# Optimization experiments

Measured on AMD Instinct MI355X. Metric: run time of the kernel, lower is better.

## Reference

```python
import jax, jax.numpy as jnp
import numpy as np
from jax import lax

D_MODEL = 512; D_FF = 2048
D_STATE = 16; D_CONV = 4; EXPAND = 2          # mamba_ssm defaults
D_INNER = EXPAND * D_MODEL                    # 1024
DT_RANK = (D_MODEL + 15) // 16                # 32
B, W, C, D = 2, 1024, 64, 8                   # C*D == D_MODEL


def setup_inputs():
    key = jax.random.key(0)
    ks = jax.random.split(key, 24)
    def p(k, shape, s=0.02):
        return jax.random.normal(k, shape, jnp.float32) * s
    inp = {"x": jax.random.normal(ks[0], (B, W, C, D), jnp.float32)}
    for i, pref in enumerate(["fm", "bm"]):
        o = 1 + i * 7
        inp[pref + "_in_W"] = p(ks[o], (2 * D_INNER, D_MODEL))
        inp[pref + "_conv_W"] = p(ks[o + 1], (D_INNER, D_CONV))
        inp[pref + "_conv_b"] = jnp.zeros((D_INNER,), jnp.float32)
        inp[pref + "_xproj_W"] = p(ks[o + 2], (DT_RANK + 2 * D_STATE, D_INNER))
        inp[pref + "_dt_W"] = p(ks[o + 3], (D_INNER, DT_RANK))
        inp[pref + "_dt_b"] = p(ks[o + 4], (D_INNER,), 0.1)
        inp[pref + "_A_log"] = jnp.log(jnp.broadcast_to(
            jnp.arange(1, D_STATE + 1, dtype=jnp.float32), (D_INNER, D_STATE)))
        inp[pref + "_D"] = jnp.ones((D_INNER,), jnp.float32)
        inp[pref + "_out_W"] = p(ks[o + 5], (D_MODEL, D_INNER))
    inp["ln1_g"] = jnp.ones((D_MODEL,), jnp.float32); inp["ln1_b"] = jnp.zeros((D_MODEL,), jnp.float32)
    inp["ln2_g"] = jnp.ones((D_MODEL,), jnp.float32); inp["ln2_b"] = jnp.zeros((D_MODEL,), jnp.float32)
    inp["ln3_g"] = jnp.ones((D_MODEL,), jnp.float32); inp["ln3_b"] = jnp.zeros((D_MODEL,), jnp.float32)
    inp["ff_W1"] = p(ks[15], (D_FF, D_MODEL)); inp["ff_b1"] = jnp.zeros((D_FF,), jnp.float32)
    inp["ff_W2"] = p(ks[16], (D_MODEL, D_FF)); inp["ff_b2"] = jnp.zeros((D_MODEL,), jnp.float32)
    return inp


def _silu(x):
    return x * jax.nn.sigmoid(x)


def _layernorm(x, g, b, eps=1e-5):
    mu = jnp.mean(x, -1, keepdims=True)
    var = jnp.var(x, -1, keepdims=True)
    return (x - mu) * lax.rsqrt(var + eps) * g + b


def _mamba(u, in_W, conv_W, conv_b, xproj_W, dt_W, dt_b, A_log, Dp, out_W):
    # u: (B, L, d_model). Standard Mamba block (mamba_ssm reference math).
    xz = jnp.einsum('bld,ed->ble', u, in_W)            # (B, L, 2*d_inner)
    xm, z = jnp.split(xz, 2, axis=-1)
    # causal depthwise conv along L
    xc = lax.conv_general_dilated(
        xm.transpose(0, 2, 1), conv_W[:, None, :], (1,),
        [(D_CONV - 1, 0)], feature_group_count=D_INNER)
    xm = _silu((xc + conv_b[None, :, None]).transpose(0, 2, 1))  # (B, L, d_inner)
    dbc = jnp.einsum('bld,ed->ble', xm, xproj_W)       # (B, L, dt_rank + 2*d_state)
    dt = dbc[..., :DT_RANK]
    Bm = dbc[..., DT_RANK:DT_RANK + D_STATE]           # (B, L, d_state)
    Cm = dbc[..., DT_RANK + D_STATE:]                  # (B, L, d_state)
    delta = jax.nn.softplus(jnp.einsum('blr,dr->bld', dt, dt_W) + dt_b)  # (B, L, d_inner)
    A = -jnp.exp(A_log)                                # (d_inner, d_state)
    dA = jnp.exp(delta[..., None] * A)                 # (B, L, d_inner, d_state)
    dBu = delta[..., None] * Bm[:, :, None, :] * xm[..., None]

    def step(h, inputs):
        dA_t, dBu_t = inputs
        h = dA_t * h + dBu_t
        return h, h

    h0 = jnp.zeros((u.shape[0], D_INNER, D_STATE), u.dtype)
    _, hs = lax.scan(step, h0, (dA.transpose(1, 0, 2, 3), dBu.transpose(1, 0, 2, 3)))
    y = jnp.einsum('lbds,lbs->bld', hs, Cm.transpose(1, 0, 2))
    y = y + xm * Dp
    y = y * _silu(z)
    return jnp.einsum('ble,de->bld', y, out_W)         # (B, L, d_model)


def reference(x,
              fm_in_W, fm_conv_W, fm_conv_b, fm_xproj_W, fm_dt_W, fm_dt_b, fm_A_log, fm_D, fm_out_W,
              bm_in_W, bm_conv_W, bm_conv_b, bm_xproj_W, bm_dt_W, bm_dt_b, bm_A_log, bm_D, bm_out_W,
              ln1_g, ln1_b, ln2_g, ln2_b, ln3_g, ln3_b,
              ff_W1, ff_b1, ff_W2, ff_b2):
    b, w, c, d = x.shape
    xf = x.reshape(b, w, c * d)
    fwd = _mamba(xf, fm_in_W, fm_conv_W, fm_conv_b, fm_xproj_W, fm_dt_W, fm_dt_b, fm_A_log, fm_D, fm_out_W)
    bwd = jnp.flip(_mamba(jnp.flip(xf, 1), bm_in_W, bm_conv_W, bm_conv_b, bm_xproj_W,
                          bm_dt_W, bm_dt_b, bm_A_log, bm_D, bm_out_W), 1)
    an1 = _layernorm(xf + fwd, ln1_g, ln1_b)   # AddNorm: LN(x + dropout(y)); dropout off at eval
    an2 = _layernorm(xf + bwd, ln2_g, ln2_b)
    out = an1 + an2
    h = jnp.maximum(jnp.einsum('bld,fd->blf', out, ff_W1) + ff_b1, 0)
    ff = jnp.einsum('blf,df->bld', h, ff_W2) + ff_b2
    out = _layernorm(ff + ff, ln3_g, ln3_b)    # an3(out, out) == LN(out + out)
    return out.reshape(b, w, c, d)
```

## Files before the change

### kernel.cpp

```cpp
#include <hip/hip_runtime.h>
#include <hip/hip_bf16.h>
#include <math.h>

#define MM 2048
#define BATCH 2
#define SEQ 1024
#define DMODEL 512
#define DINNER 1024
#define DSTATE 16
#define DTRANK 32
#define DFF 2048

#define NCHUNK 16
#define CHUNK 64
#define GTOT 65536

typedef short bf16x8 __attribute__((ext_vector_type(8)));
typedef float floatx4 __attribute__((ext_vector_type(4)));
typedef unsigned short ushort8v __attribute__((ext_vector_type(8)));
typedef unsigned short ushort4v __attribute__((ext_vector_type(4)));

__device__ __forceinline__ unsigned short f2bf(float f) {
    union { float f; unsigned u; } v; v.f = f;
    unsigned r = v.u + 0x7FFF + ((v.u >> 16) & 1);
    return (unsigned short)(r >> 16);
}
__device__ __forceinline__ float bf2f(unsigned short u) {
    union { unsigned u; float f; } v; v.u = ((unsigned)u) << 16; return v.f;
}

__device__ __forceinline__ float rowsum16(float x) {
    union { float f; int i; } a, b;
    a.f = x;
    b.i = __builtin_amdgcn_update_dpp(0, a.i, 0x128, 0xF, 0xF, false); a.f += b.f;
    b.i = __builtin_amdgcn_update_dpp(0, a.i, 0x124, 0xF, 0xF, false); a.f += b.f;
    b.i = __builtin_amdgcn_update_dpp(0, a.i, 0x122, 0xF, 0xF, false); a.f += b.f;
    b.i = __builtin_amdgcn_update_dpp(0, a.i, 0x121, 0xF, 0xF, false); a.f += b.f;
    return a.f;
}

#define GLOAD_LDS16(gp, lp) __builtin_amdgcn_global_load_lds( \
    (const __attribute__((address_space(1))) unsigned int*)(gp), \
    (__attribute__((address_space(3))) unsigned int*)(lp), 16, 0, 0)

template<int EPI, int OUTBF16>
__global__ __launch_bounds__(256) void gemm_mfma_batch(
    int M, int N, int K,
    const unsigned short* __restrict__ A0, const unsigned short* __restrict__ A1, int lda,
    const unsigned short* __restrict__ B0, const unsigned short* __restrict__ B1, int ldb,
    const float* __restrict__ bias,
    void* __restrict__ C0, void* __restrict__ C1, int ldc)
{
    __shared__ unsigned short As[128 * 32];
    __shared__ unsigned short Bs[128 * 32];
    const int z = blockIdx.z;
    const unsigned short* A = z ? A1 : A0;
    const unsigned short* B = z ? B1 : B0;
    void* Cout = z ? C1 : C0;
    const int tid  = threadIdx.x;
    const int wave = tid >> 6;
    const int lane = tid & 63;
    const int bm = blockIdx.y * 128;
    const int bn = blockIdx.x * 128;

    const int strow = lane & 15;
    const int stkc  = lane >> 4;
    const int wr = wave >> 1, wc = wave & 1;
    const int frow = lane & 15;
    const int fkc  = lane >> 4;

    floatx4 acc[4][4];
    #pragma unroll
    for (int i = 0; i < 4; ++i)
        #pragma unroll
        for (int j = 0; j < 4; ++j)
            acc[i][j] = (floatx4){0.f, 0.f, 0.f, 0.f};

    for (int k0 = 0; k0 < K; k0 += 32) {
        __syncthreads();
        #pragma unroll
        for (int q = 0; q < 2; ++q) {
            int g = wave * 2 + q;
            GLOAD_LDS16(A + (size_t)(bm + g * 16 + strow) * lda + k0 + stkc * 8,
                        As + g * 512);
        }
        #pragma unroll
        for (int q = 0; q < 2; ++q) {
            int g = wave * 2 + q;
            GLOAD_LDS16(B + (size_t)(bn + g * 16 + strow) * ldb + k0 + stkc * 8,
                        Bs + g * 512);
        }
        __syncthreads();

        bf16x8 af[4], bfr[4];
        #pragma unroll
        for (int i = 0; i < 4; ++i)
            af[i] = *(const bf16x8*)(As + (wr * 4 + i) * 512 + fkc * 128 + frow * 8);
        #pragma unroll
        for (int j = 0; j < 4; ++j)
            bfr[j] = *(const bf16x8*)(Bs + (wc * 4 + j) * 512 + fkc * 128 + frow * 8);
        #pragma unroll
        for (int i = 0; i < 4; ++i)
            #pragma unroll
            for (int j = 0; j < 4; ++j)
                acc[i][j] = __builtin_amdgcn_mfma_f32_16x16x32_bf16(
                    af[i], bfr[j], acc[i][j], 0, 0, 0);
    }

    const int orow0 = bm + wr * 64 + (lane >> 4) * 4;
    const int ocol0 = bn + wc * 64 + (lane & 15);
    #pragma unroll
    for (int j = 0; j < 4; ++j) {
        const int col = ocol0 + j * 16;
        const float bv = bias ? bias[col] : 0.f;
        #pragma unroll
        for (int i = 0; i < 4; ++i) {
            #pragma unroll
            for (int r = 0; r < 4; ++r) {
                int row = orow0 + i * 16 + r;
                float t = acc[i][j][r] + bv;
                if (EPI == 1) t = fmaxf(t, 0.f);
                if (OUTBF16)
                    ((unsigned short*)Cout)[(size_t)row * ldc + col] = f2bf(t);
                else
                    ((float*)Cout)[(size_t)row * ldc + col] = t;
            }
        }
    }
}

__global__ __launch_bounds__(256) void gemm_inproj_kernel(
    const unsigned short* __restrict__ A,
    const unsigned short* __restrict__ B0, const unsigned short* __restrict__ B1,
    float* __restrict__ Cx0, float* __restrict__ Cz0,
    float* __restrict__ Cx1, float* __restrict__ Cz1)
{
    __shared__ unsigned short As[128 * 32];
    __shared__ unsigned short Bs[128 * 32];
    const int z = blockIdx.z;
    const unsigned short* B = z ? B1 : B0;
    const int tid  = threadIdx.x;
    const int wave = tid >> 6;
    const int lane = tid & 63;
    const int bm = blockIdx.y * 128;
    const int bn = blockIdx.x * 128;

    const int strow = lane & 15;
    const int stkc  = lane >> 4;
    const int wr = wave >> 1, wc = wave & 1;
    const int frow = lane & 15;
    const int fkc  = lane >> 4;

    floatx4 acc[4][4];
    #pragma unroll
    for (int i = 0; i < 4; ++i)
        #pragma unroll
        for (int j = 0; j < 4; ++j)
            acc[i][j] = (floatx4){0.f, 0.f, 0.f, 0.f};

    for (int k0 = 0; k0 < DMODEL; k0 += 32) {
        __syncthreads();
        #pragma unroll
        for (int q = 0; q < 2; ++q) {
            int g = wave * 2 + q;
            GLOAD_LDS16(A + (size_t)(bm + g * 16 + strow) * DMODEL + k0 + stkc * 8,
                        As + g * 512);
        }
        #pragma unroll
        for (int q = 0; q < 2; ++q) {
            int g = wave * 2 + q;
            GLOAD_LDS16(B + (size_t)(bn + g * 16 + strow) * DMODEL + k0 + stkc * 8,
                        Bs + g * 512);
        }
        __syncthreads();

        bf16x8 af[4], bfr[4];
        #pragma unroll
        for (int i = 0; i < 4; ++i)
            af[i] = *(const bf16x8*)(As + (wr * 4 + i) * 512 + fkc * 128 + frow * 8);
        #pragma unroll
        for (int j = 0; j < 4; ++j)
            bfr[j] = *(const bf16x8*)(Bs + (wc * 4 + j) * 512 + fkc * 128 + frow * 8);
        #pragma unroll
        for (int i = 0; i < 4; ++i)
            #pragma unroll
            for (int j = 0; j < 4; ++j)
                acc[i][j] = __builtin_amdgcn_mfma_f32_16x16x32_bf16(
                    af[i], bfr[j], acc[i][j], 0, 0, 0);
    }

    const int zh = bn >= DINNER;
    float* C = z ? (zh ? Cz1 : Cx1) : (zh ? Cz0 : Cx0);
    const int cb = zh ? DINNER : 0;
    const int orow0 = bm + wr * 64 + (lane >> 4) * 4;
    const int ocol0 = bn + wc * 64 + (lane & 15) - cb;
    #pragma unroll
    for (int j = 0; j < 4; ++j) {
        const int col = ocol0 + j * 16;
        #pragma unroll
        for (int i = 0; i < 4; ++i)
            #pragma unroll
            for (int r = 0; r < 4; ++r)
                C[(size_t)(orow0 + i * 16 + r) * DINNER + col] = acc[i][j][r];
    }
}

template<int NSPLIT>
__global__ __launch_bounds__(256) void gemm_mfma_splitk(
    int M, int N, int K,
    const unsigned short* __restrict__ A0, const unsigned short* __restrict__ A1, int lda,
    const unsigned short* __restrict__ B0, const unsigned short* __restrict__ B1, int ldb,
    float* __restrict__ part, int ldc)
{
    __shared__ unsigned short As[128 * 32];
    __shared__ unsigned short Bs[128 * 32];
    const int z = blockIdx.z;
    const int dir = z / NSPLIT, sp = z % NSPLIT;
    const unsigned short* A = dir ? A1 : A0;
    const unsigned short* B = dir ? B1 : B0;
    float* Cp = part + (size_t)z * M * ldc;
    const int kbeg = sp * (K / NSPLIT);
    const int kend = kbeg + (K / NSPLIT);
    const int tid  = threadIdx.x;
    const int wave = tid >> 6;
    const int lane = tid & 63;
    const int bm = blockIdx.y * 128;
    const int bn = blockIdx.x * 128;

    const int strow = lane & 15;
    const int stkc  = lane >> 4;
    const int wr = wave >> 1, wc = wave & 1;
    const int frow = lane & 15;
    const int fkc  = lane >> 4;

    floatx4 acc[4][4];
    #pragma unroll
    for (int i = 0; i < 4; ++i)
        #pragma unroll
        for (int j = 0; j < 4; ++j)
            acc[i][j] = (floatx4){0.f, 0.f, 0.f, 0.f};

    for (int k0 = kbeg; k0 < kend; k0 += 32) {
        __syncthreads();
        #pragma unroll
        for (int q = 0; q < 2; ++q) {
            int g = wave * 2 + q;
            GLOAD_LDS16(A + (size_t)(bm + g * 16 + strow) * lda + k0 + stkc * 8,
                        As + g * 512);
        }
        #pragma unroll
        for (int q = 0; q < 2; ++q) {
            int g = wave * 2 + q;
            GLOAD_LDS16(B + (size_t)(bn + g * 16 + strow) * ldb + k0 + stkc * 8,
                        Bs + g * 512);
        }
        __syncthreads();

        bf16x8 af[4], bfr[4];
        #pragma unroll
        for (int i = 0; i < 4; ++i)
            af[i] = *(const bf16x8*)(As + (wr * 4 + i) * 512 + fkc * 128 + frow * 8);
        #pragma unroll
        for (int j = 0; j < 4; ++j)
            bfr[j] = *(const bf16x8*)(Bs + (wc * 4 + j) * 512 + fkc * 128 + frow * 8);
        #pragma unroll
        for (int i = 0; i < 4; ++i)
            #pragma unroll
            for (int j = 0; j < 4; ++j)
                acc[i][j] = __builtin_amdgcn_mfma_f32_16x16x32_bf16(
                    af[i], bfr[j], acc[i][j], 0, 0, 0);
    }

    const int orow0 = bm + wr * 64 + (lane >> 4) * 4;
    const int ocol0 = bn + wc * 64 + (lane & 15);
    #pragma unroll
    for (int j = 0; j < 4; ++j) {
        const int col = ocol0 + j * 16;
        #pragma unroll
        for (int i = 0; i < 4; ++i)
            #pragma unroll
            for (int r = 0; r < 4; ++r)
                Cp[(size_t)(orow0 + i * 16 + r) * ldc + col] = acc[i][j][r];
    }
}

__global__ __launch_bounds__(256) void reduce_splitk_kernel(
    const float* __restrict__ part, int nsplit, int elems, int ldc,
    const float* __restrict__ bias, float* __restrict__ out)
{
    int i = (blockIdx.x * 256 + threadIdx.x) * 4;
    if (i >= elems) return;
    float4 a = *(const float4*)(part + i);
    for (int s = 1; s < nsplit; ++s) {
        float4 t = *(const float4*)(part + (size_t)s * elems + i);
        a.x += t.x; a.y += t.y; a.z += t.z; a.w += t.w;
    }
    if (bias) {
        int c = i % ldc;
        a.x += bias[c]; a.y += bias[c + 1]; a.z += bias[c + 2]; a.w += bias[c + 3];
    }
    *(float4*)(out + i) = a;
}

__global__ __launch_bounds__(256) void reduce_splitk2_dual_kernel(
    const float* __restrict__ part, float* __restrict__ out0, float* __restrict__ out1)
{
    const int dir = blockIdx.y;
    const int i = (blockIdx.x * 256 + threadIdx.x) * 4;
    const float* p = part + (size_t)dir * 2 * (MM * DMODEL);
    float4 a = *(const float4*)(p + i);
    float4 t = *(const float4*)(p + (size_t)(MM * DMODEL) + i);
    a.x += t.x; a.y += t.y; a.z += t.z; a.w += t.w;
    float* out = dir ? out1 : out0;
    *(float4*)(out + i) = a;
}

__global__ __launch_bounds__(256) void xproj_splitk_kernel(
    const unsigned short* __restrict__ A_f, const unsigned short* __restrict__ A_b,
    const unsigned short* __restrict__ Wf,  const unsigned short* __restrict__ Wb,
    float* __restrict__ part)
{
    __shared__ unsigned short As[128 * 32];
    __shared__ unsigned short Bs[64 * 32];
    const int tid = threadIdx.x, wave = tid >> 6, lane = tid & 63;
    const int bm = blockIdx.x * 128;
    const int dir = blockIdx.y >> 2, sp = blockIdx.y & 3;
    const unsigned short* A = dir ? A_b : A_f;
    const unsigned short* W = dir ? Wb  : Wf;
    float* Cp = part + (size_t)blockIdx.y * MM * 64;
    const int kbeg = sp * 256, kend = kbeg + 256;

    const int strow = lane & 15;
    const int stkc  = lane >> 4;
    const int frow = lane & 15;
    const int fkc  = lane >> 4;

    floatx4 acc[2][4];
    #pragma unroll
    for (int i = 0; i < 2; ++i)
        #pragma unroll
        for (int j = 0; j < 4; ++j)
            acc[i][j] = (floatx4){0.f, 0.f, 0.f, 0.f};

    for (int k0 = kbeg; k0 < kend; k0 += 32) {
        __syncthreads();
        #pragma unroll
        for (int q = 0; q < 2; ++q) {
            int g = wave * 2 + q;
            GLOAD_LDS16(A + (size_t)(bm + g * 16 + strow) * DINNER + k0 + stkc * 8,
                        As + g * 512);
        }
        GLOAD_LDS16(W + (size_t)(wave * 16 + strow) * DINNER + k0 + stkc * 8,
                    Bs + wave * 512);
        __syncthreads();

        bf16x8 af[2], bfr[4];
        #pragma unroll
        for (int i = 0; i < 2; ++i)
            af[i] = *(const bf16x8*)(As + (wave * 2 + i) * 512 + fkc * 128 + frow * 8);
        #pragma unroll
        for (int j = 0; j < 4; ++j)
            bfr[j] = *(const bf16x8*)(Bs + j * 512 + fkc * 128 + frow * 8);
        #pragma unroll
        for (int i = 0; i < 2; ++i)
            #pragma unroll
            for (int j = 0; j < 4; ++j)
                acc[i][j] = __builtin_amdgcn_mfma_f32_16x16x32_bf16(
                    af[i], bfr[j], acc[i][j], 0, 0, 0);
    }

    const int orow0 = bm + wave * 32 + (lane >> 4) * 4;
    #pragma unroll
    for (int j = 0; j < 4; ++j) {
        const int col = (lane & 15) + j * 16;
        #pragma unroll
        for (int i = 0; i < 2; ++i)
            #pragma unroll
            for (int r = 0; r < 4; ++r)
                Cp[(size_t)(orow0 + i * 16 + r) * 64 + col] = acc[i][j][r];
    }
}

__global__ __launch_bounds__(256) void xproj_reduce_kernel(
    const float* __restrict__ part,
    float* __restrict__ dbc_f, float* __restrict__ dbc_b,
    float* __restrict__ dbcT_f, float* __restrict__ dbcT_b)
{
    const int dir = blockIdx.y;
    const int i = (blockIdx.x * 256 + threadIdx.x) * 4;
    const float* p = part + (size_t)dir * 4 * (MM * 64);
    float4 a = *(const float4*)(p + i);
    #pragma unroll
    for (int s = 1; s < 4; ++s) {
        float4 t = *(const float4*)(p + (size_t)s * (MM * 64) + i);
        a.x += t.x; a.y += t.y; a.z += t.z; a.w += t.w;
    }
    float* dbc  = dir ? dbc_b  : dbc_f;
    float* dbcT = dir ? dbcT_b : dbcT_f;
    *(float4*)(dbc + i) = a;
    const int m = i >> 6, c = i & 63;
    dbcT[(size_t)(c + 0) * MM + m] = a.x;
    dbcT[(size_t)(c + 1) * MM + m] = a.y;
    dbcT[(size_t)(c + 2) * MM + m] = a.z;
    dbcT[(size_t)(c + 3) * MM + m] = a.w;
}

__global__ __launch_bounds__(256) void dtproj_batch_kernel(
    int M, int N, int K,
    const float* __restrict__ A0, const float* __restrict__ A1, int lda,
    const float* __restrict__ B0, const float* __restrict__ B1, int ldb,
    const float* __restrict__ bias0, const float* __restrict__ bias1,
    unsigned short* __restrict__ C0, unsigned short* __restrict__ C1, int ldc)
{
    __shared__ float As[16][64];
    __shared__ float Bs[16][64];
    const int z = blockIdx.z;
    const float* A = z ? A1 : A0;
    const float* B = z ? B1 : B0;
    const float* biasR = z ? bias1 : bias0;
    unsigned short* C = z ? C1 : C0;
    const int tid = threadIdx.x;
    const int tx = tid & 15, ty = tid >> 4;
    const int bm = blockIdx.y * 64, bn = blockIdx.x * 64;
    const int lm = tid & 63;
    const int lk = (tid >> 6) * 4;
    const float* Arow = A + (size_t)(bm + lm) * lda + lk;
    const float* Brow = B + (size_t)(bn + lm) * ldb + lk;
    float acc[4][4] = {};
    for (int k0 = 0; k0 < K; k0 += 16) {
        float4 av = *(const float4*)(Arow + k0);
        float4 bv = *(const float4*)(Brow + k0);
        __syncthreads();
        As[lk+0][lm] = av.x; As[lk+1][lm] = av.y; As[lk+2][lm] = av.z; As[lk+3][lm] = av.w;
        Bs[lk+0][lm] = bv.x; Bs[lk+1][lm] = bv.y; Bs[lk+2][lm] = bv.z; Bs[lk+3][lm] = bv.w;
        __syncthreads();
        #pragma unroll
        for (int k = 0; k < 16; ++k) {
            float4 a = *(const float4*)(&As[k][ty*4]);
            float4 b = *(const float4*)(&Bs[k][tx*4]);
            float ar[4] = {a.x,a.y,a.z,a.w};
            float br[4] = {b.x,b.y,b.z,b.w};
            #pragma unroll
            for (int i = 0; i < 4; ++i)
                #pragma unroll
                for (int j = 0; j < 4; ++j)
                    acc[i][j] = fmaf(ar[i], br[j], acc[i][j]);
        }
    }
    const int row0 = bm + ty*4, col0 = bn + tx*4;
    #pragma unroll
    for (int i = 0; i < 4; ++i) {
        float br = biasR[row0 + i];
        ushort4v o;
        #pragma unroll
        for (int j = 0; j < 4; ++j) {
            float t = acc[i][j] + br;
            o[j] = f2bf(fmaxf(t, 0.f) + log1pf(__expf(-fabsf(t))));
        }
        *(ushort4v*)(C + (size_t)(row0 + i) * ldc + col0) = o;
    }
}

__global__ __launch_bounds__(256) void cast_pre_kernel(
    const float* __restrict__ x, const float* __restrict__ w0,
    const float* __restrict__ w1, const float* __restrict__ xp0,
    const float* __restrict__ xp1, unsigned short* __restrict__ dst)
{
    int i = (blockIdx.x * 256 + threadIdx.x) * 8;
    const float* src; int off;
    if      (i < 1048576) { src = x;   off = 0; }
    else if (i < 2097152) { src = w0;  off = 1048576; }
    else if (i < 3145728) { src = w1;  off = 2097152; }
    else if (i < 3211264) { src = xp0; off = 3145728; }
    else                  { src = xp1; off = 3211264; }
    float4 a = *(const float4*)(src + i - off);
    float4 b = *(const float4*)(src + i - off + 4);
    ushort8v o;
    o[0] = f2bf(a.x); o[1] = f2bf(a.y); o[2] = f2bf(a.z); o[3] = f2bf(a.w);
    o[4] = f2bf(b.x); o[5] = f2bf(b.y); o[6] = f2bf(b.z); o[7] = f2bf(b.w);
    *(ushort8v*)(dst + i) = o;
}

__global__ __launch_bounds__(256) void cast_post_kernel(
    const float* __restrict__ w0, const float* __restrict__ w1,
    const float* __restrict__ w2, const float* __restrict__ w3,
    unsigned short* __restrict__ dst)
{
    int i = (blockIdx.x * 256 + threadIdx.x) * 8;
    const float* src; int off;
    if      (i < 524288)  { src = w0; off = 0; }
    else if (i < 1048576) { src = w1; off = 524288; }
    else if (i < 2097152) { src = w2; off = 1048576; }
    else                  { src = w3; off = 2097152; }
    float4 a = *(const float4*)(src + i - off);
    float4 b = *(const float4*)(src + i - off + 4);
    ushort8v o;
    o[0] = f2bf(a.x); o[1] = f2bf(a.y); o[2] = f2bf(a.z); o[3] = f2bf(a.w);
    o[4] = f2bf(b.x); o[5] = f2bf(b.y); o[6] = f2bf(b.z); o[7] = f2bf(b.w);
    *(ushort8v*)(dst + i) = o;
}

__global__ __launch_bounds__(256) void conv_silu_kernel(
    const float* __restrict__ x_f, const float* __restrict__ x_b,
    const float* __restrict__ Wf,  const float* __restrict__ Wb,
    const float* __restrict__ cbf, const float* __restrict__ cbb,
    unsigned short* __restrict__ of, unsigned short* __restrict__ ob)
{
    const int dir = blockIdx.y;
    const float* xo = dir ? x_b : x_f;
    const float* convW = dir ? Wb : Wf;
    const float* convb = dir ? cbb : cbf;
    unsigned short* xm_bf = dir ? ob : of;
    int gid = blockIdx.x * 256 + threadIdx.x;
    int c = gid & (DINNER - 1);
    int m = gid >> 10;
    int b = m >> 10;
    int l = m & (SEQ - 1);
    float4 wv = *(const float4*)(convW + c * 4);
    float w[4] = {wv.x, wv.y, wv.z, wv.w};
    float acc = convb[c];
    #pragma unroll
    for (int j = 0; j < 4; ++j) {
        int p = dir ? (l + 3 - j) : (l - 3 + j);
        if (p >= 0 && p < SEQ)
            acc = fmaf(xo[(size_t)(b * SEQ + p) * DINNER + c], w[j], acc);
    }
    float sig = 1.f / (1.f + __expf(-acc));
    xm_bf[(size_t)m * DINNER + c] = f2bf(acc * sig);
}

__global__ __launch_bounds__(256) void transpose_bf16_kernel(
    const unsigned short* __restrict__ in0, const unsigned short* __restrict__ in1,
    unsigned short* __restrict__ out0, unsigned short* __restrict__ out1,
    int R, int C)
{
    __shared__ unsigned short t[32][34];
    const unsigned short* in = blockIdx.z ? in1 : in0;
    unsigned short* out = blockIdx.z ? out1 : out0;
    const int c0 = blockIdx.x * 32, r0 = blockIdx.y * 32;
    const int tx = threadIdx.x & 31, ty = threadIdx.x >> 5;
    #pragma unroll
    for (int rr = 0; rr < 32; rr += 8)
        t[ty + rr][tx] = in[(size_t)(r0 + ty + rr) * C + c0 + tx];
    __syncthreads();
    #pragma unroll
    for (int rr = 0; rr < 32; rr += 8)
        out[(size_t)(c0 + ty + rr) * R + r0 + tx] = t[tx][ty + rr];
}

template<int DIR>
__device__ __forceinline__ void pass1_body(
    const unsigned short* __restrict__ deltaT, const unsigned short* __restrict__ xmT,
    const float* __restrict__ dbcT, const float* __restrict__ Alog,
    const float* __restrict__ Dv,
    float* __restrict__ y0T, float* __restrict__ cumT,
    float* __restrict__ Pout, float* __restrict__ Hout)
{
    const int tid = threadIdx.x;
    const int s = tid & 15;
    const int dloc = tid >> 4;
    const int d = blockIdx.x * 16 + dloc;
    const int b = blockIdx.y / NCHUNK;
    const int c = blockIdx.y % NCHUNK;

    const float A  = -__expf(Alog[d * DSTATE + s]);
    const float Dp = Dv[d];
    const unsigned short* dRow = deltaT + (size_t)d * MM + b * SEQ;
    const unsigned short* xRow = xmT + (size_t)d * MM + b * SEQ;
    const float* bRow = dbcT + (size_t)(DTRANK + s) * MM + b * SEQ;
    const float* cRow = dbcT + (size_t)(DTRANK + DSTATE + s) * MM + b * SEQ;
    float* yRow = y0T + (size_t)d * MM + b * SEQ;
    float* uRow = cumT + (size_t)d * MM + b * SEQ;

    float h = 0.f, sdl = 0.f;
    const int segBase = DIR ? (SEQ - CHUNK - c * CHUNK) : (c * CHUNK);
    for (int ii = 0; ii < CHUNK; ii += 8) {
        const int off = DIR ? (segBase + (CHUNK - 8) - ii) : (segBase + ii);
        ushort8v dl8 = *(const ushort8v*)(dRow + off);
        ushort8v x8  = *(const ushort8v*)(xRow + off);
        float4 b0 = *(const float4*)(bRow + off);
        float4 b1 = *(const float4*)(bRow + off + 4);
        float4 c0 = *(const float4*)(cRow + off);
        float4 c1 = *(const float4*)(cRow + off + 4);
        float Bv[8] = {b0.x,b0.y,b0.z,b0.w,b1.x,b1.y,b1.z,b1.w};
        float Cv[8] = {c0.x,c0.y,c0.z,c0.w,c1.x,c1.y,c1.z,c1.w};
        float yv[8], cu[8];
        #pragma unroll
        for (int u = 0; u < 8; ++u) {
            const int t = DIR ? (7 - u) : u;
            float dlv = bf2f(dl8[t]);
            float xv  = bf2f(x8[t]);
            float dA = __expf(dlv * A);
            sdl += dlv;
            h = fmaf(dA, h, dlv * Bv[t] * xv);
            float part = rowsum16(h * Cv[t]);
            yv[t] = fmaf(xv, Dp, part);
            cu[t] = sdl;
        }
        if (s == 0) {
            *(float4*)(yRow + off)     = (float4){yv[0], yv[1], yv[2], yv[3]};
            *(float4*)(yRow + off + 4) = (float4){yv[4], yv[5], yv[6], yv[7]};
            *(float4*)(uRow + off)     = (float4){cu[0], cu[1], cu[2], cu[3]};
            *(float4*)(uRow + off + 4) = (float4){cu[4], cu[5], cu[6], cu[7]};
        }
    }
    const int g = ((DIR * BATCH + b) * DINNER + d) * DSTATE + s;
    Pout[(size_t)c * GTOT + g] = __expf(sdl * A);
    Hout[(size_t)c * GTOT + g] = h;
}

__global__ __launch_bounds__(256) void scan_pass1_kernel(
    const unsigned short* __restrict__ dT_f, const unsigned short* __restrict__ dT_b,
    const unsigned short* __restrict__ xT_f, const unsigned short* __restrict__ xT_b,
    const float* __restrict__ dbcT_f, const float* __restrict__ dbcT_b,
    const float* __restrict__ Alog_f, const float* __restrict__ Alog_b,
    const float* __restrict__ D_f, const float* __restrict__ D_b,
    float* __restrict__ y0T_f, float* __restrict__ y0T_b,
    float* __restrict__ cumT_f, float* __restrict__ cumT_b,
    float* __restrict__ Pout, float* __restrict__ Hout)
{
    if (blockIdx.z == 0)
        pass1_body<0>(dT_f, xT_f, dbcT_f, Alog_f, D_f, y0T_f, cumT_f, Pout, Hout);
    else
        pass1_body<1>(dT_b, xT_b, dbcT_b, Alog_b, D_b, y0T_b, cumT_b, Pout, Hout);
}

__global__ __launch_bounds__(256) void scan_carry_kernel(
    const float* __restrict__ P, const float* __restrict__ H,
    float* __restrict__ carry)
{
    const int g = blockIdx.x * 256 + threadIdx.x;
    float h = 0.f;
    #pragma unroll
    for (int c = 0; c < NCHUNK; ++c) {
        carry[(size_t)c * GTOT + g] = h;
        h = fmaf(P[(size_t)c * GTOT + g], h, H[(size_t)c * GTOT + g]);
    }
}

__global__ __launch_bounds__(256) void scan_correct_kernel(
    const float* __restrict__ y0T_f, const float* __restrict__ y0T_b,
    const float* __restrict__ cumT_f, const float* __restrict__ cumT_b,
    const float* __restrict__ dbcT_f, const float* __restrict__ dbcT_b,
    const float* __restrict__ Alog_f, const float* __restrict__ Alog_b,
    const float* __restrict__ carry,
    const float* __restrict__ z_f, const float* __restrict__ z_b,
    unsigned short* __restrict__ ybf_f, unsigned short* __restrict__ ybf_b)
{
    __shared__ float Cs[16][33];
    __shared__ float Asm[32][16];
    __shared__ float Cy[32][16];
    __shared__ float t[32][33];

    const int dir = blockIdx.z;
    const float* y0T  = dir ? y0T_b  : y0T_f;
    const float* cumT = dir ? cumT_b : cumT_f;
    const float* dbcT = dir ? dbcT_b : dbcT_f;
    const float* Alog = dir ? Alog_b : Alog_f;
    const float* zon  = dir ? z_b    : z_f;
    unsigned short* ybf = dir ? ybf_b : ybf_f;

    const int m0 = blockIdx.x * 32, d0 = blockIdx.y * 32;
    const int b = m0 >> 10;
    const int l0 = m0 & (SEQ - 1);
    const int c = dir ? ((SEQ - 1 - l0) >> 6) : (l0 >> 6);

    for (int idx = threadIdx.x; idx < 512; idx += 256) {
        int s = idx >> 5, ml = idx & 31;
        Cs[s][ml] = dbcT[(size_t)(DTRANK + DSTATE + s) * MM + m0 + ml];
        int dl2 = idx >> 4, s2 = idx & 15;
        Asm[dl2][s2] = -__expf(Alog[(d0 + dl2) * DSTATE + s2]);
        Cy[dl2][s2] = carry[(size_t)c * GTOT
            + ((size_t)(dir * BATCH + b) * DINNER + d0 + dl2) * DSTATE + s2];
    }
    __syncthreads();

    const int tx = threadIdx.x & 31, ty = threadIdx.x >> 5;
    #pragma unroll
    for (int rr = 0; rr < 32; rr += 8) {
        const int dloc = ty + rr;
        const size_t base = (size_t)(d0 + dloc) * MM + m0 + tx;
        float u  = cumT[base];
        float y0 = y0T[base];
        float corr = 0.f;
        #pragma unroll
        for (int s = 0; s < DSTATE; ++s)
            corr = fmaf(Cs[s][tx] * Cy[dloc][s], __expf(Asm[dloc][s] * u), corr);
        t[dloc][tx] = y0 + corr;
    }
    __syncthreads();
    #pragma unroll
    for (int rr = 0; rr < 32; rr += 8) {
        int m = m0 + ty + rr, d = d0 + tx;
        float z = zon[(size_t)m * DINNER + d];
        float sig = 1.f / (1.f + __expf(-z));
        ybf[(size_t)m * DINNER + d] = f2bf(t[tx][ty + rr] * (z * sig));
    }
}

__global__ __launch_bounds__(256) void ln_combine_kernel(
    const float* __restrict__ xf,
    const float* __restrict__ pf, const float* __restrict__ pb,
    const float* __restrict__ g1, const float* __restrict__ b1,
    const float* __restrict__ g2, const float* __restrict__ b2,
    unsigned short* __restrict__ out)
{
    const int m = blockIdx.x;
    const int tid = threadIdx.x;
    const float* xr = xf + (size_t)m * DMODEL;
    const float* p1 = pf + (size_t)m * DMODEL;
    const float* p2 = pb + (size_t)m * DMODEL;
    float v1a = xr[tid] + p1[tid];
    float v1b = xr[tid + 256] + p1[tid + 256];
    float v2a = xr[tid] + p2[tid];
    float v2b = xr[tid + 256] + p2[tid + 256];
    float s1 = v1a + v1b, q1 = v1a*v1a + v1b*v1b;
    float s2 = v2a + v2b, q2 = v2a*v2a + v2b*v2b;
    #pragma unroll
    for (int off = 32; off; off >>= 1) {
        s1 += __shfl_xor(s1, off); q1 += __shfl_xor(q1, off);
        s2 += __shfl_xor(s2, off); q2 += __shfl_xor(q2, off);
    }
    __shared__ float sm[4][4];
    const int w = tid >> 6;
    if ((tid & 63) == 0) { sm[w][0] = s1; sm[w][1] = q1; sm[w][2] = s2; sm[w][3] = q2; }
    __syncthreads();
    s1 = sm[0][0] + sm[1][0] + sm[2][0] + sm[3][0];
    q1 = sm[0][1] + sm[1][1] + sm[2][1] + sm[3][1];
    s2 = sm[0][2] + sm[1][2] + sm[2][2] + sm[3][2];
    q2 = sm[0][3] + sm[1][3] + sm[2][3] + sm[3][3];
    const float inv = 1.f / DMODEL;
    float mu1 = s1 * inv, mu2 = s2 * inv;
    float rs1 = rsqrtf(q1 * inv - mu1 * mu1 + 1e-5f);
    float rs2 = rsqrtf(q2 * inv - mu2 * mu2 + 1e-5f);
    unsigned short* orow = out + (size_t)m * DMODEL;
    orow[tid]       = f2bf((v1a - mu1) * rs1 * g1[tid]       + b1[tid]
                         + (v2a - mu2) * rs2 * g2[tid]       + b2[tid]);
    orow[tid + 256] = f2bf((v1b - mu1) * rs1 * g1[tid + 256] + b1[tid + 256]
                         + (v2b - mu2) * rs2 * g2[tid + 256] + b2[tid + 256]);
}

__global__ __launch_bounds__(256) void ln_final_kernel(
    const float* __restrict__ ff,
    const float* __restrict__ g, const float* __restrict__ b,
    float* __restrict__ out)
{
    const int m = blockIdx.x;
    const int tid = threadIdx.x;
    const float* fr = ff + (size_t)m * DMODEL;
    float va = 2.f * fr[tid];
    float vb = 2.f * fr[tid + 256];
    float s = va + vb, q = va*va + vb*vb;
    #pragma unroll
    for (int off = 32; off; off >>= 1) {
        s += __shfl_xor(s, off); q += __shfl_xor(q, off);
    }
    __shared__ float sm[4][2];
    const int w = tid >> 6;
    if ((tid & 63) == 0) { sm[w][0] = s; sm[w][1] = q; }
    __syncthreads();
    s = sm[0][0] + sm[1][0] + sm[2][0] + sm[3][0];
    q = sm[0][1] + sm[1][1] + sm[2][1] + sm[3][1];
    const float inv = 1.f / DMODEL;
    float mu = s * inv;
    float rs = rsqrtf(q * inv - mu * mu + 1e-5f);
    float* orow = out + (size_t)m * DMODEL;
    orow[tid]       = (va - mu) * rs * g[tid]       + b[tid];
    orow[tid + 256] = (vb - mu) * rs * g[tid + 256] + b[tid + 256];
}

extern "C" void kernel_launch(void* const* d_in, const int* in_sizes, int n_in,
                              void* d_out, int out_size, void* d_ws, size_t ws_size,
                              hipStream_t stream)
{
    const float* x         = (const float*)d_in[0];
    const float* fm_in_W   = (const float*)d_in[1];
    const float* fm_conv_W = (const float*)d_in[2];
    const float* fm_conv_b = (const float*)d_in[3];
    const float* fm_xproj_W= (const float*)d_in[4];
    const float* fm_dt_W   = (const float*)d_in[5];
    const float* fm_dt_b   = (const float*)d_in[6];
    const float* fm_A_log  = (const float*)d_in[7];
    const float* fm_D      = (const float*)d_in[8];
    const float* fm_out_W  = (const float*)d_in[9];
    const float* bm_in_W   = (const float*)d_in[10];
    const float* bm_conv_W = (const float*)d_in[11];
    const float* bm_conv_b = (const float*)d_in[12];
    const float* bm_xproj_W= (const float*)d_in[13];
    const float* bm_dt_W   = (const float*)d_in[14];
    const float* bm_dt_b   = (const float*)d_in[15];
    const float* bm_A_log  = (const float*)d_in[16];
    const float* bm_D      = (const float*)d_in[17];
    const float* bm_out_W  = (const float*)d_in[18];
    const float* ln1_g     = (const float*)d_in[19];
    const float* ln1_b     = (const float*)d_in[20];
    const float* ln2_g     = (const float*)d_in[21];
    const float* ln2_b     = (const float*)d_in[22];
    const float* ln3_g     = (const float*)d_in[23];
    const float* ln3_b     = (const float*)d_in[24];
    const float* ff_W1     = (const float*)d_in[25];
    const float* ff_b1     = (const float*)d_in[26];
    const float* ff_W2     = (const float*)d_in[27];
    const float* ff_b2     = (const float*)d_in[28];
    float* out = (float*)d_out;

    float* ws = (float*)d_ws;
    size_t o = 0;
    float* xonly_f = ws + o; o += (size_t)MM * DINNER;
    float* xonly_b = ws + o; o += (size_t)MM * DINNER;
    float* zonly_f = ws + o; o += (size_t)MM * DINNER;
    float* zonly_b = ws + o; o += (size_t)MM * DINNER;
    unsigned short* xm_bf_f = (unsigned short*)(ws + o); o += (size_t)MM * DINNER / 2;
    unsigned short* xm_bf_b = (unsigned short*)(ws + o); o += (size_t)MM * DINNER / 2;
    unsigned short* xmT_f   = (unsigned short*)(ws + o); o += (size_t)MM * DINNER / 2;
    unsigned short* xmT_b   = (unsigned short*)(ws + o); o += (size_t)MM * DINNER / 2;
    unsigned short* deltaT_f= (unsigned short*)(ws + o); o += (size_t)MM * DINNER / 2;
    unsigned short* deltaT_b= (unsigned short*)(ws + o); o += (size_t)MM * DINNER / 2;
    float* dbc_f    = ws + o; o += (size_t)MM * 64;
    float* dbc_b    = ws + o; o += (size_t)MM * 64;
    float* dbcT_f   = ws + o; o += (size_t)MM * 64;
    float* dbcT_b   = ws + o; o += (size_t)MM * 64;
    float* y0T_f    = ws + o; o += (size_t)MM * DINNER;
    float* y0T_b    = ws + o; o += (size_t)MM * DINNER;
    float* scanP    = ws + o; o += (size_t)NCHUNK * (GTOT / 16) * 16;
    float* scanH    = ws + o; o += (size_t)NCHUNK * (GTOT / 16) * 16;
    float* scanCy   = ws + o; o += (size_t)NCHUNK * (GTOT / 16) * 16;

    float* cumT_f = xonly_f;
    float* cumT_b = xonly_b;
    unsigned short* x_bf       = (unsigned short*)scanP;
    unsigned short* fm_inW_bf  = x_bf + 1048576;
    unsigned short* bm_inW_bf  = fm_inW_bf + 1048576;
    unsigned short* fm_xpW_bf  = bm_inW_bf + 1048576;
    unsigned short* bm_xpW_bf  = fm_xpW_bf + 65536;
    float* gpartX = y0T_f;
    unsigned short* ybf_f = (unsigned short*)scanP;
    unsigned short* ybf_b = (unsigned short*)scanH;
    unsigned short* fm_outW_bf = (unsigned short*)zonly_f;
    unsigned short* bm_outW_bf = fm_outW_bf + 524288;
    unsigned short* W1_bf      = bm_outW_bf + 524288;
    unsigned short* W2_bf      = W1_bf + 1048576;
    float* gpartO = y0T_f;
    float* proj_f = scanCy;
    float* proj_b = xonly_f;
    unsigned short* outsum_bf  = (unsigned short*)xonly_b;
    unsigned short* h_bf = (unsigned short*)deltaT_f;
    float* ff2 = scanP;

    cast_pre_kernel<<<3276800 / 2048, 256, 0, stream>>>(
        x, fm_in_W, bm_in_W, fm_xproj_W, bm_xproj_W, x_bf);

    gemm_inproj_kernel<<<dim3(2048/128, MM/128, 2), 256, 0, stream>>>(
        x_bf, fm_inW_bf, bm_inW_bf, xonly_f, zonly_f, xonly_b, zonly_b);

    conv_silu_kernel<<<dim3((MM * DINNER) / 256, 2), 256, 0, stream>>>(
        xonly_f, xonly_b, fm_conv_W, bm_conv_W, fm_conv_b, bm_conv_b, xm_bf_f, xm_bf_b);
    transpose_bf16_kernel<<<dim3(DINNER/32, MM/32, 2), 256, 0, stream>>>(
        xm_bf_f, xm_bf_b, xmT_f, xmT_b, MM, DINNER);

    xproj_splitk_kernel<<<dim3(MM/128, 8), 256, 0, stream>>>(
        xm_bf_f, xm_bf_b, fm_xpW_bf, bm_xpW_bf, gpartX);
    xproj_reduce_kernel<<<dim3((MM*64)/1024, 2), 256, 0, stream>>>(
        gpartX, dbc_f, dbc_b, dbcT_f, dbcT_b);

    dtproj_batch_kernel<<<dim3(MM/64, DINNER/64, 2), 256, 0, stream>>>(
        DINNER, MM, DTRANK, fm_dt_W, bm_dt_W, DTRANK, dbc_f, dbc_b, 64,
        fm_dt_b, bm_dt_b, deltaT_f, deltaT_b, MM);

    scan_pass1_kernel<<<dim3(DINNER/16, BATCH*NCHUNK, 2), 256, 0, stream>>>(
        deltaT_f, deltaT_b, xmT_f, xmT_b, dbcT_f, dbcT_b,
        fm_A_log, bm_A_log, fm_D, bm_D,
        y0T_f, y0T_b, cumT_f, cumT_b, scanP, scanH);
    scan_carry_kernel<<<GTOT/256, 256, 0, stream>>>(scanP, scanH, scanCy);
    scan_correct_kernel<<<dim3(MM/32, DINNER/32, 2), 256, 0, stream>>>(
        y0T_f, y0T_b, cumT_f, cumT_b, dbcT_f, dbcT_b, fm_A_log, bm_A_log,
        scanCy, zonly_f, zonly_b, ybf_f, ybf_b);

    cast_post_kernel<<<3145728 / 2048, 256, 0, stream>>>(
        fm_out_W, bm_out_W, ff_W1, ff_W2, fm_outW_bf);

    gemm_mfma_splitk<2><<<dim3(DMODEL/128, MM/128, 4), 256, 0, stream>>>(
        MM, DMODEL, DINNER, ybf_f, ybf_b, DINNER, fm_outW_bf, bm_outW_bf, DINNER,
        gpartO, DMODEL);
    reduce_splitk2_dual_kernel<<<dim3((MM*DMODEL)/1024, 2), 256, 0, stream>>>(
        gpartO, proj_f, proj_b);

    ln_combine_kernel<<<MM, 256, 0, stream>>>(
        x, proj_f, proj_b, ln1_g, ln1_b, ln2_g, ln2_b, outsum_bf);

    gemm_mfma_batch<1,1><<<dim3(DFF/128, MM/128, 1), 256, 0, stream>>>(
        MM, DFF, DMODEL, outsum_bf, outsum_bf, DMODEL, W1_bf, W1_bf, DMODEL,
        ff_b1, h_bf, h_bf, DFF);

    gemm_mfma_splitk<4><<<dim3(DMODEL/128, MM/128, 4), 256, 0, stream>>>(
        MM, DMODEL, DFF, h_bf, h_bf, DFF, W2_bf, W2_bf, DFF, gpartO, DMODEL);
    reduce_splitk_kernel<<<(MM*DMODEL)/1024, 256, 0, stream>>>(
        gpartO, 4, MM*DMODEL, DMODEL, ff_b2, ff2);

    ln_final_kernel<<<MM, 256, 0, stream>>>(ff2, ln3_g, ln3_b, out);
}
```

Baseline: 365.1 us.

## Fuse split-K reductions into layernorms, store y0 as bf16, repack B/C row-major

Both split-K reduce kernels are removed. The layernorm kernels now sum the partial GEMM outputs directly from a dedicated workspace, which saves two launches and a full write and read of the intermediate. The x-proj reduce writes delta-rank and B/C as separate row-major arrays instead of a strided transposed copy, so the scan kernels read B/C per timestep with stride 32. The scan's intermediate y0 is also stored in bf16 to halve that traffic, at some cost in precision.

```diff
diff --git a/kernel.cpp b/kernel.cpp
--- a/kernel.cpp
+++ b/kernel.cpp
@@ -284,37 +284,6 @@
     }
 }
 
-__global__ __launch_bounds__(256) void reduce_splitk_kernel(
-    const float* __restrict__ part, int nsplit, int elems, int ldc,
-    const float* __restrict__ bias, float* __restrict__ out)
-{
-    int i = (blockIdx.x * 256 + threadIdx.x) * 4;
-    if (i >= elems) return;
-    float4 a = *(const float4*)(part + i);
-    for (int s = 1; s < nsplit; ++s) {
-        float4 t = *(const float4*)(part + (size_t)s * elems + i);
-        a.x += t.x; a.y += t.y; a.z += t.z; a.w += t.w;
-    }
-    if (bias) {
-        int c = i % ldc;
-        a.x += bias[c]; a.y += bias[c + 1]; a.z += bias[c + 2]; a.w += bias[c + 3];
-    }
-    *(float4*)(out + i) = a;
-}
-
-__global__ __launch_bounds__(256) void reduce_splitk2_dual_kernel(
-    const float* __restrict__ part, float* __restrict__ out0, float* __restrict__ out1)
-{
-    const int dir = blockIdx.y;
-    const int i = (blockIdx.x * 256 + threadIdx.x) * 4;
-    const float* p = part + (size_t)dir * 2 * (MM * DMODEL);
-    float4 a = *(const float4*)(p + i);
-    float4 t = *(const float4*)(p + (size_t)(MM * DMODEL) + i);
-    a.x += t.x; a.y += t.y; a.z += t.z; a.w += t.w;
-    float* out = dir ? out1 : out0;
-    *(float4*)(out + i) = a;
-}
-
 __global__ __launch_bounds__(256) void xproj_splitk_kernel(
     const unsigned short* __restrict__ A_f, const unsigned short* __restrict__ A_b,
     const unsigned short* __restrict__ Wf,  const unsigned short* __restrict__ Wb,
@@ -384,7 +353,7 @@
 __global__ __launch_bounds__(256) void xproj_reduce_kernel(
     const float* __restrict__ part,
     float* __restrict__ dbc_f, float* __restrict__ dbc_b,
-    float* __restrict__ dbcT_f, float* __restrict__ dbcT_b)
+    float* __restrict__ bct_f, float* __restrict__ bct_b)
 {
     const int dir = blockIdx.y;
     const int i = (blockIdx.x * 256 + threadIdx.x) * 4;
@@ -395,14 +364,14 @@
         float4 t = *(const float4*)(p + (size_t)s * (MM * 64) + i);
         a.x += t.x; a.y += t.y; a.z += t.z; a.w += t.w;
     }
-    float* dbc  = dir ? dbc_b  : dbc_f;
-    float* dbcT = dir ? dbcT_b : dbcT_f;
-    *(float4*)(dbc + i) = a;
     const int m = i >> 6, c = i & 63;
-    dbcT[(size_t)(c + 0) * MM + m] = a.x;
-    dbcT[(size_t)(c + 1) * MM + m] = a.y;
-    dbcT[(size_t)(c + 2) * MM + m] = a.z;
-    dbcT[(size_t)(c + 3) * MM + m] = a.w;
+    if (c < 32) {
+        float* dbc = dir ? dbc_b : dbc_f;
+        *(float4*)(dbc + (size_t)m * 32 + c) = a;
+    } else {
+        float* bct = dir ? bct_b : bct_f;
+        *(float4*)(bct + (size_t)m * 32 + (c - 32)) = a;
+    }
 }
 
 __global__ __launch_bounds__(256) void dtproj_batch_kernel(
@@ -551,9 +520,9 @@
 template<int DIR>
 __device__ __forceinline__ void pass1_body(
     const unsigned short* __restrict__ deltaT, const unsigned short* __restrict__ xmT,
-    const float* __restrict__ dbcT, const float* __restrict__ Alog,
+    const float* __restrict__ bct, const float* __restrict__ Alog,
     const float* __restrict__ Dv,
-    float* __restrict__ y0T, float* __restrict__ cumT,
+    unsigned short* __restrict__ y0T, float* __restrict__ cumT,
     float* __restrict__ Pout, float* __restrict__ Hout)
 {
     const int tid = threadIdx.x;
@@ -567,9 +536,8 @@
     const float Dp = Dv[d];
     const unsigned short* dRow = deltaT + (size_t)d * MM + b * SEQ;
     const unsigned short* xRow = xmT + (size_t)d * MM + b * SEQ;
-    const float* bRow = dbcT + (size_t)(DTRANK + s) * MM + b * SEQ;
-    const float* cRow = dbcT + (size_t)(DTRANK + DSTATE + s) * MM + b * SEQ;
-    float* yRow = y0T + (size_t)d * MM + b * SEQ;
+    const float* bcRow = bct + (size_t)(b * SEQ) * 32 + s;
+    unsigned short* yRow = y0T + (size_t)d * MM + b * SEQ;
     float* uRow = cumT + (size_t)d * MM + b * SEQ;
 
     float h = 0.f, sdl = 0.f;
@@ -578,12 +546,13 @@
         const int off = DIR ? (segBase + (CHUNK - 8) - ii) : (segBase + ii);
         ushort8v dl8 = *(const ushort8v*)(dRow + off);
         ushort8v x8  = *(const ushort8v*)(xRow + off);
-        float4 b0 = *(const float4*)(bRow + off);
-        float4 b1 = *(const float4*)(bRow + off + 4);
-        float4 c0 = *(const float4*)(cRow + off);
-        float4 c1 = *(const float4*)(cRow + off + 4);
-        float Bv[8] = {b0.x,b0.y,b0.z,b0.w,b1.x,b1.y,b1.z,b1.w};
-        float Cv[8] = {c0.x,c0.y,c0.z,c0.w,c1.x,c1.y,c1.z,c1.w};
+        const float* bp = bcRow + (size_t)off * 32;
+        float Bv[8], Cv[8];
+        #pragma unroll
+        for (int u = 0; u < 8; ++u) {
+            Bv[u] = bp[u * 32];
+            Cv[u] = bp[u * 32 + 16];
+        }
         float yv[8], cu[8];
         #pragma unroll
         for (int u = 0; u < 8; ++u) {
@@ -598,8 +567,10 @@
             cu[t] = sdl;
         }
         if (s == 0) {
-            *(float4*)(yRow + off)     = (float4){yv[0], yv[1], yv[2], yv[3]};
-            *(float4*)(yRow + off + 4) = (float4){yv[4], yv[5], yv[6], yv[7]};
+            ushort8v y8;
+            #pragma unroll
+            for (int u = 0; u < 8; ++u) y8[u] = f2bf(yv[u]);
+            *(ushort8v*)(yRow + off) = y8;
             *(float4*)(uRow + off)     = (float4){cu[0], cu[1], cu[2], cu[3]};
             *(float4*)(uRow + off + 4) = (float4){cu[4], cu[5], cu[6], cu[7]};
         }
@@ -612,17 +583,17 @@
 __global__ __launch_bounds__(256) void scan_pass1_kernel(
     const unsigned short* __restrict__ dT_f, const unsigned short* __restrict__ dT_b,
     const unsigned short* __restrict__ xT_f, const unsigned short* __restrict__ xT_b,
-    const float* __restrict__ dbcT_f, const float* __restrict__ dbcT_b,
+    const float* __restrict__ bct_f, const float* __restrict__ bct_b,
     const float* __restrict__ Alog_f, const float* __restrict__ Alog_b,
     const float* __restrict__ D_f, const float* __restrict__ D_b,
-    float* __restrict__ y0T_f, float* __restrict__ y0T_b,
+    unsigned short* __restrict__ y0T_f, unsigned short* __restrict__ y0T_b,
     float* __restrict__ cumT_f, float* __restrict__ cumT_b,
     float* __restrict__ Pout, float* __restrict__ Hout)
 {
     if (blockIdx.z == 0)
-        pass1_body<0>(dT_f, xT_f, dbcT_f, Alog_f, D_f, y0T_f, cumT_f, Pout, Hout);
+        pass1_body<0>(dT_f, xT_f, bct_f, Alog_f, D_f, y0T_f, cumT_f, Pout, Hout);
     else
-        pass1_body<1>(dT_b, xT_b, dbcT_b, Alog_b, D_b, y0T_b, cumT_b, Pout, Hout);
+        pass1_body<1>(dT_b, xT_b, bct_b, Alog_b, D_b, y0T_b, cumT_b, Pout, Hout);
 }
 
 __global__ __launch_bounds__(256) void scan_carry_kernel(
@@ -639,9 +610,9 @@
 }
 
 __global__ __launch_bounds__(256) void scan_correct_kernel(
-    const float* __restrict__ y0T_f, const float* __restrict__ y0T_b,
+    const unsigned short* __restrict__ y0T_f, const unsigned short* __restrict__ y0T_b,
     const float* __restrict__ cumT_f, const float* __restrict__ cumT_b,
-    const float* __restrict__ dbcT_f, const float* __restrict__ dbcT_b,
+    const float* __restrict__ bct_f, const float* __restrict__ bct_b,
     const float* __restrict__ Alog_f, const float* __restrict__ Alog_b,
     const float* __restrict__ carry,
     const float* __restrict__ z_f, const float* __restrict__ z_b,
@@ -653,9 +624,9 @@
     __shared__ float t[32][33];
 
     const int dir = blockIdx.z;
-    const float* y0T  = dir ? y0T_b  : y0T_f;
+    const unsigned short* y0T = dir ? y0T_b : y0T_f;
     const float* cumT = dir ? cumT_b : cumT_f;
-    const float* dbcT = dir ? dbcT_b : dbcT_f;
+    const float* bct  = dir ? bct_b  : bct_f;
     const float* Alog = dir ? Alog_b : Alog_f;
     const float* zon  = dir ? z_b    : z_f;
     unsigned short* ybf = dir ? ybf_b : ybf_f;
@@ -666,8 +637,8 @@
     const int c = dir ? ((SEQ - 1 - l0) >> 6) : (l0 >> 6);
 
     for (int idx = threadIdx.x; idx < 512; idx += 256) {
-        int s = idx >> 5, ml = idx & 31;
-        Cs[s][ml] = dbcT[(size_t)(DTRANK + DSTATE + s) * MM + m0 + ml];
+        int s1 = idx & 15, ml = idx >> 4;
+        Cs[s1][ml] = bct[(size_t)(m0 + ml) * 32 + 16 + s1];
         int dl2 = idx >> 4, s2 = idx & 15;
         Asm[dl2][s2] = -__expf(Alog[(d0 + dl2) * DSTATE + s2]);
         Cy[dl2][s2] = carry[(size_t)c * GTOT
@@ -681,7 +652,7 @@
         const int dloc = ty + rr;
         const size_t base = (size_t)(d0 + dloc) * MM + m0 + tx;
         float u  = cumT[base];
-        float y0 = y0T[base];
+        float y0 = bf2f(y0T[base]);
         float corr = 0.f;
         #pragma unroll
         for (int s = 0; s < DSTATE; ++s)
@@ -698,9 +669,8 @@
     }
 }
 
-__global__ __launch_bounds__(256) void ln_combine_kernel(
-    const float* __restrict__ xf,
-    const float* __restrict__ pf, const float* __restrict__ pb,
+__global__ __launch_bounds__(256) void ln_combine_fused_kernel(
+    const float* __restrict__ xf, const float* __restrict__ part,
     const float* __restrict__ g1, const float* __restrict__ b1,
     const float* __restrict__ g2, const float* __restrict__ b2,
     unsigned short* __restrict__ out)
@@ -708,12 +678,14 @@
     const int m = blockIdx.x;
     const int tid = threadIdx.x;
     const float* xr = xf + (size_t)m * DMODEL;
-    const float* p1 = pf + (size_t)m * DMODEL;
-    const float* p2 = pb + (size_t)m * DMODEL;
-    float v1a = xr[tid] + p1[tid];
-    float v1b = xr[tid + 256] + p1[tid + 256];
-    float v2a = xr[tid] + p2[tid];
-    float v2b = xr[tid + 256] + p2[tid + 256];
+    const float* p0 = part + (size_t)m * DMODEL;
+    const float* p1 = p0 + (size_t)MM * DMODEL;
+    const float* p2 = p1 + (size_t)MM * DMODEL;
+    const float* p3 = p2 + (size_t)MM * DMODEL;
+    float v1a = xr[tid]       + p0[tid]       + p1[tid];
+    float v1b = xr[tid + 256] + p0[tid + 256] + p1[tid + 256];
+    float v2a = xr[tid]       + p2[tid]       + p3[tid];
+    float v2b = xr[tid + 256] + p2[tid + 256] + p3[tid + 256];
     float s1 = v1a + v1b, q1 = v1a*v1a + v1b*v1b;
     float s2 = v2a + v2b, q2 = v2a*v2a + v2b*v2b;
     #pragma unroll
@@ -740,16 +712,20 @@
                          + (v2b - mu2) * rs2 * g2[tid + 256] + b2[tid + 256]);
 }
 
-__global__ __launch_bounds__(256) void ln_final_kernel(
-    const float* __restrict__ ff,
+__global__ __launch_bounds__(256) void ln_final_fused_kernel(
+    const float* __restrict__ part, const float* __restrict__ bias,
     const float* __restrict__ g, const float* __restrict__ b,
     float* __restrict__ out)
 {
     const int m = blockIdx.x;
     const int tid = threadIdx.x;
-    const float* fr = ff + (size_t)m * DMODEL;
-    float va = 2.f * fr[tid];
-    float vb = 2.f * fr[tid + 256];
+    const size_t stride = (size_t)MM * DMODEL;
+    const float* p = part + (size_t)m * DMODEL;
+    float fa = bias[tid]       + p[tid]       + p[stride + tid]
+             + p[2*stride + tid]       + p[3*stride + tid];
+    float fb = bias[tid + 256] + p[tid + 256] + p[stride + tid + 256]
+             + p[2*stride + tid + 256] + p[3*stride + tid + 256];
+    float va = 2.f * fa, vb = 2.f * fb;
     float s = va + vb, q = va*va + vb*vb;
     #pragma unroll
     for (int off = 32; off; off >>= 1) {
@@ -816,15 +792,16 @@
     unsigned short* xmT_b   = (unsigned short*)(ws + o); o += (size_t)MM * DINNER / 2;
     unsigned short* deltaT_f= (unsigned short*)(ws + o); o += (size_t)MM * DINNER / 2;
     unsigned short* deltaT_b= (unsigned short*)(ws + o); o += (size_t)MM * DINNER / 2;
-    float* dbc_f    = ws + o; o += (size_t)MM * 64;
-    float* dbc_b    = ws + o; o += (size_t)MM * 64;
-    float* dbcT_f   = ws + o; o += (size_t)MM * 64;
-    float* dbcT_b   = ws + o; o += (size_t)MM * 64;
-    float* y0T_f    = ws + o; o += (size_t)MM * DINNER;
-    float* y0T_b    = ws + o; o += (size_t)MM * DINNER;
+    float* dbc_f    = ws + o; o += (size_t)MM * 32;
+    float* dbc_b    = ws + o; o += (size_t)MM * 32;
+    float* bct_f    = ws + o; o += (size_t)MM * 32;
+    float* bct_b    = ws + o; o += (size_t)MM * 32;
+    unsigned short* y0T_f = (unsigned short*)(ws + o); o += (size_t)MM * DINNER / 2;
+    unsigned short* y0T_b = (unsigned short*)(ws + o); o += (size_t)MM * DINNER / 2;
     float* scanP    = ws + o; o += (size_t)NCHUNK * (GTOT / 16) * 16;
     float* scanH    = ws + o; o += (size_t)NCHUNK * (GTOT / 16) * 16;
     float* scanCy   = ws + o; o += (size_t)NCHUNK * (GTOT / 16) * 16;
+    float* gpart    = ws + o; o += (size_t)4 * MM * DMODEL;
 
     float* cumT_f = xonly_f;
     float* cumT_b = xonly_b;
@@ -833,19 +810,14 @@
     unsigned short* bm_inW_bf  = fm_inW_bf + 1048576;
     unsigned short* fm_xpW_bf  = bm_inW_bf + 1048576;
     unsigned short* bm_xpW_bf  = fm_xpW_bf + 65536;
-    float* gpartX = y0T_f;
     unsigned short* ybf_f = (unsigned short*)scanP;
     unsigned short* ybf_b = (unsigned short*)scanH;
     unsigned short* fm_outW_bf = (unsigned short*)zonly_f;
     unsigned short* bm_outW_bf = fm_outW_bf + 524288;
     unsigned short* W1_bf      = bm_outW_bf + 524288;
     unsigned short* W2_bf      = W1_bf + 1048576;
-    float* gpartO = y0T_f;
-    float* proj_f = scanCy;
-    float* proj_b = xonly_f;
     unsigned short* outsum_bf  = (unsigned short*)xonly_b;
     unsigned short* h_bf = (unsigned short*)deltaT_f;
-    float* ff2 = scanP;
 
     cast_pre_kernel<<<3276800 / 2048, 256, 0, stream>>>(
         x, fm_in_W, bm_in_W, fm_xproj_W, bm_xproj_W, x_bf);
@@ -859,21 +831,21 @@
         xm_bf_f, xm_bf_b, xmT_f, xmT_b, MM, DINNER);
 
     xproj_splitk_kernel<<<dim3(MM/128, 8), 256, 0, stream>>>(
-        xm_bf_f, xm_bf_b, fm_xpW_bf, bm_xpW_bf, gpartX);
+        xm_bf_f, xm_bf_b, fm_xpW_bf, bm_xpW_bf, gpart);
     xproj_reduce_kernel<<<dim3((MM*64)/1024, 2), 256, 0, stream>>>(
-        gpartX, dbc_f, dbc_b, dbcT_f, dbcT_b);
+        gpart, dbc_f, dbc_b, bct_f, bct_b);
 
     dtproj_batch_kernel<<<dim3(MM/64, DINNER/64, 2), 256, 0, stream>>>(
-        DINNER, MM, DTRANK, fm_dt_W, bm_dt_W, DTRANK, dbc_f, dbc_b, 64,
+        DINNER, MM, DTRANK, fm_dt_W, bm_dt_W, DTRANK, dbc_f, dbc_b, 32,
         fm_dt_b, bm_dt_b, deltaT_f, deltaT_b, MM);
 
     scan_pass1_kernel<<<dim3(DINNER/16, BATCH*NCHUNK, 2), 256, 0, stream>>>(
-        deltaT_f, deltaT_b, xmT_f, xmT_b, dbcT_f, dbcT_b,
+        deltaT_f, deltaT_b, xmT_f, xmT_b, bct_f, bct_b,
         fm_A_log, bm_A_log, fm_D, bm_D,
         y0T_f, y0T_b, cumT_f, cumT_b, scanP, scanH);
     scan_carry_kernel<<<GTOT/256, 256, 0, stream>>>(scanP, scanH, scanCy);
     scan_correct_kernel<<<dim3(MM/32, DINNER/32, 2), 256, 0, stream>>>(
-        y0T_f, y0T_b, cumT_f, cumT_b, dbcT_f, dbcT_b, fm_A_log, bm_A_log,
+        y0T_f, y0T_b, cumT_f, cumT_b, bct_f, bct_b, fm_A_log, bm_A_log,
         scanCy, zonly_f, zonly_b, ybf_f, ybf_b);
 
     cast_post_kernel<<<3145728 / 2048, 256, 0, stream>>>(
@@ -881,21 +853,18 @@
 
     gemm_mfma_splitk<2><<<dim3(DMODEL/128, MM/128, 4), 256, 0, stream>>>(
         MM, DMODEL, DINNER, ybf_f, ybf_b, DINNER, fm_outW_bf, bm_outW_bf, DINNER,
-        gpartO, DMODEL);
-    reduce_splitk2_dual_kernel<<<dim3((MM*DMODEL)/1024, 2), 256, 0, stream>>>(
-        gpartO, proj_f, proj_b);
-
-    ln_combine_kernel<<<MM, 256, 0, stream>>>(
-        x, proj_f, proj_b, ln1_g, ln1_b, ln2_g, ln2_b, outsum_bf);
+        gpart, DMODEL);
+
+    ln_combine_fused_kernel<<<MM, 256, 0, stream>>>(
+        x, gpart, ln1_g, ln1_b, ln2_g, ln2_b, outsum_bf);
 
     gemm_mfma_batch<1,1><<<dim3(DFF/128, MM/128, 1), 256, 0, stream>>>(
         MM, DFF, DMODEL, outsum_bf, outsum_bf, DMODEL, W1_bf, W1_bf, DMODEL,
         ff_b1, h_bf, h_bf, DFF);
 
     gemm_mfma_splitk<4><<<dim3(DMODEL/128, MM/128, 4), 256, 0, stream>>>(
-        MM, DMODEL, DFF, h_bf, h_bf, DFF, W2_bf, W2_bf, DFF, gpartO, DMODEL);
-    reduce_splitk_kernel<<<(MM*DMODEL)/1024, 256, 0, stream>>>(
-        gpartO, 4, MM*DMODEL, DMODEL, ff_b2, ff2);
-
-    ln_final_kernel<<<MM, 256, 0, stream>>>(ff2, ln3_g, ln3_b, out);
-}
+        MM, DMODEL, DFF, h_bf, h_bf, DFF, W2_bf, W2_bf, DFF, gpart, DMODEL);
+
+    ln_final_fused_kernel<<<MM, 256, 0, stream>>>(
+        gpart, ff_b2, ln3_g, ln3_b, out);
+}
```

Result: faster. 335.6 us (-8.1%).
